# Kernel optimization log

Hardware: AMD Instinct MI355X
Metric: run time of the kernel (lower is better)

## Reference

```python
import jax, jax.numpy as jnp
import numpy as np

B, N, D, H, IN, HID = 16, 1024, 256, 8, 256, 1024
HD = IN // H  # head dim = 32
EPS = 1e-5


def layer_norm(x, g, b):
    mu = jnp.mean(x, axis=-1, keepdims=True)
    var = jnp.var(x, axis=-1, keepdims=True)
    return (x - mu) / jnp.sqrt(var + EPS) * g + b


def setup_inputs() -> dict:
    key = jax.random.key(0)
    ks = jax.random.split(key, 12)
    s = 0.02
    return {
        "x": jax.random.normal(ks[0], (B, N, D), jnp.float32),
        "coords": jax.random.normal(ks[1], (B, N, 2), jnp.float32),
        "g1": jnp.ones((D,), jnp.float32),
        "b1": jnp.zeros((D,), jnp.float32),
        "Wqkv": jax.random.normal(ks[2], (3 * IN, D), jnp.float32) * s,
        "Wproj": jax.random.normal(ks[3], (IN, IN), jnp.float32) * s,
        "bproj": jnp.zeros((IN,), jnp.float32),
        "g2": jnp.ones((D,), jnp.float32),
        "b2": jnp.zeros((D,), jnp.float32),
        "W1": jax.random.normal(ks[4], (HID, D), jnp.float32) * s,
        "bb1": jnp.zeros((HID,), jnp.float32),
        "W2": jax.random.normal(ks[5], (D, HID), jnp.float32) * s,
        "bb2": jnp.zeros((D,), jnp.float32),
    }


def reference(x, coords, g1, b1, Wqkv, Wproj, bproj, g2, b2, W1, bb1, W2, bb2):
    # ---- Attention branch (pre-norm) ----
    h = layer_norm(x, g1, b1)                       # [B,N,D]
    qkv = h @ Wqkv.T                                # [B,N,3*IN]
    qkv = qkv.reshape(B, N, 3, H, HD).transpose(2, 0, 3, 1, 4)  # [3,B,H,N,HD]
    q, k, v = qkv[0], qkv[1], qkv[2]
    scale = HD ** -0.5
    attn = jnp.einsum('bhid,bhjd->bhij', q * scale, k)  # [B,H,N,N]
    attn = jax.nn.softmax(attn, axis=-1)
    o = jnp.einsum('bhij,bhjd->bhid', attn, v)      # [B,H,N,HD]
    o = o.transpose(0, 2, 1, 3).reshape(B, N, IN)   # [B,N,IN]
    o = o @ Wproj.T + bproj
    o = o + h                                       # residual inside Attention (vs normed input)
    x = x + o                                       # Block residual (double residual, faithful)
    # ---- MLP branch ----
    h2 = layer_norm(x, g2, b2)
    m = jax.nn.gelu(h2 @ W1.T + bb1, approximate=False) @ W2.T + bb2
    return x + m
```

## Files before the change

kernel.cpp:

```cpp
#include <hip/hip_runtime.h>
#include <hip/hip_bf16.h>
#include <math.h>

#define Bdim 16
#define Ndim 1024
#define Ddim 256
#define Hdim 8
#define HDdim 32
#define INdim 256
#define HIDdim 1024
#define Tdim (Bdim * Ndim)

typedef __attribute__((ext_vector_type(8)))  short bf16x8;
typedef __attribute__((ext_vector_type(4)))  short bf16x4;
typedef __attribute__((ext_vector_type(16))) float f32x16;
typedef unsigned int u32;

__device__ inline short f2bf(float x) {
    union { __hip_bfloat16 b; short s; } u;
    u.b = __float2bfloat16(x);
    return u.s;
}

__device__ inline float bf2f(short s) {
    return __uint_as_float(((u32)(unsigned short)s) << 16);
}

__device__ inline float fexp2(float x) {
#if __has_builtin(__builtin_amdgcn_exp2f)
    return __builtin_amdgcn_exp2f(x);
#else
    return exp2f(x);
#endif
}

__device__ inline u32 pack2bf(float a, float b) {
#if __has_builtin(__builtin_amdgcn_cvt_pk_bf16_f32)
    typedef __attribute__((ext_vector_type(2))) __bf16 bf16x2_t;
    union { bf16x2_t v; u32 u; } c;
    c.v = __builtin_amdgcn_cvt_pk_bf16_f32(a, b);
    return c.u;
#else
    u32 ua = __float_as_uint(a), ub = __float_as_uint(b);
    return ((ua + 0x8000u) >> 16) | ((ub + 0x8000u) & 0xffff0000u);
#endif
}

__device__ inline void plswap(u32 &a, u32 &b) {
    asm volatile("v_permlane32_swap_b32 %0, %1" : "+v"(a), "+v"(b));
}

__device__ inline float gelu_exact(float v) {
    return 0.5f * v * (1.0f + erff(v * 0.70710678118654752f));
}

typedef __attribute__((address_space(1))) const u32 gas_t;
typedef __attribute__((address_space(3))) u32 las_t;
__device__ inline void gl16(const short* g, short* l) {
    __builtin_amdgcn_global_load_lds((gas_t*)g, (las_t*)l, 16, 0, 0);
}

#define N4_QKV  (3 * INdim * Ddim / 4)
#define N4_PROJ (INdim * INdim / 4)
#define N4_W1   (HIDdim * Ddim / 4)
#define N4_W2   (Ddim * HIDdim / 4)
#define NCVT_BLK ((N4_QKV + N4_PROJ + N4_W1 + N4_W2) / 256)

__global__ __launch_bounds__(256) void cvt_ln1_kernel(const float* __restrict__ s0,
                                                      const float* __restrict__ s1,
                                                      const float* __restrict__ s2,
                                                      const float* __restrict__ s3,
                                                      short* __restrict__ d0,
                                                      short* __restrict__ d1,
                                                      short* __restrict__ d2,
                                                      short* __restrict__ d3,
                                                      const float* __restrict__ x,
                                                      const float* __restrict__ g,
                                                      const float* __restrict__ b,
                                                      float* __restrict__ outf,
                                                      short* __restrict__ outb) {
    const int bid = blockIdx.x;
    if (bid < NCVT_BLK) {
        int i = bid * 256 + threadIdx.x;
        const float* src; short* dst; int j;
        if (i < N4_QKV)                          { src = s0; dst = d0; j = i; }
        else if (i < N4_QKV + N4_PROJ)           { src = s1; dst = d1; j = i - N4_QKV; }
        else if (i < N4_QKV + N4_PROJ + N4_W1)   { src = s2; dst = d2; j = i - N4_QKV - N4_PROJ; }
        else                                     { src = s3; dst = d3; j = i - N4_QKV - N4_PROJ - N4_W1; }
        float4 v = ((const float4*)src)[j];
        bf16x4 bb;
        bb[0] = f2bf(v.x); bb[1] = f2bf(v.y); bb[2] = f2bf(v.z); bb[3] = f2bf(v.w);
        ((bf16x4*)dst)[j] = bb;
    } else {
        int w = threadIdx.x >> 6, lane = threadIdx.x & 63;
        int row = (bid - NCVT_BLK) * 4 + w;
        float4 v = ((const float4*)x)[(size_t)row * 64 + lane];
        float s  = (v.x + v.y) + (v.z + v.w);
        float s2 = (v.x * v.x + v.y * v.y) + (v.z * v.z + v.w * v.w);
        #pragma unroll
        for (int off = 32; off; off >>= 1) {
            s  += __shfl_xor(s,  off, 64);
            s2 += __shfl_xor(s2, off, 64);
        }
        float mu   = s * (1.0f / Ddim);
        float var  = s2 * (1.0f / Ddim) - mu * mu;
        float rstd = rsqrtf(var + 1e-5f);
        float4 gg = ((const float4*)g)[lane];
        float4 bb = ((const float4*)b)[lane];
        float4 r;
        r.x = (v.x - mu) * rstd * gg.x + bb.x;
        r.y = (v.y - mu) * rstd * gg.y + bb.y;
        r.z = (v.z - mu) * rstd * gg.z + bb.z;
        r.w = (v.w - mu) * rstd * gg.w + bb.w;
        if (outf) ((float4*)outf)[(size_t)row * 64 + lane] = r;
        bf16x4 rb;
        rb[0] = f2bf(r.x); rb[1] = f2bf(r.y); rb[2] = f2bf(r.z); rb[3] = f2bf(r.w);
        ((bf16x4*)outb)[(size_t)row * 64 + lane] = rb;
    }
}

__global__ __launch_bounds__(256) void ln4_kernel(const float* __restrict__ x,
                                                  const float* __restrict__ g,
                                                  const float* __restrict__ b,
                                                  float* __restrict__ outf,
                                                  short* __restrict__ outb) {
    int w = threadIdx.x >> 6, lane = threadIdx.x & 63;
    int row = blockIdx.x * 4 + w;
    float4 v = ((const float4*)x)[(size_t)row * 64 + lane];
    float s  = (v.x + v.y) + (v.z + v.w);
    float s2 = (v.x * v.x + v.y * v.y) + (v.z * v.z + v.w * v.w);
    #pragma unroll
    for (int off = 32; off; off >>= 1) {
        s  += __shfl_xor(s,  off, 64);
        s2 += __shfl_xor(s2, off, 64);
    }
    float mu   = s * (1.0f / Ddim);
    float var  = s2 * (1.0f / Ddim) - mu * mu;
    float rstd = rsqrtf(var + 1e-5f);
    float4 gg = ((const float4*)g)[lane];
    float4 bb = ((const float4*)b)[lane];
    float4 r;
    r.x = (v.x - mu) * rstd * gg.x + bb.x;
    r.y = (v.y - mu) * rstd * gg.y + bb.y;
    r.z = (v.z - mu) * rstd * gg.z + bb.z;
    r.w = (v.w - mu) * rstd * gg.w + bb.w;
    if (outf) ((float4*)outf)[(size_t)row * 64 + lane] = r;
    bf16x4 rb;
    rb[0] = f2bf(r.x); rb[1] = f2bf(r.y); rb[2] = f2bf(r.z); rb[3] = f2bf(r.w);
    ((bf16x4*)outb)[(size_t)row * 64 + lane] = rb;
}

#define EPI_NONE 0
#define EPI_PROJ 1
#define EPI_GELU 2
#define EPI_RES  3
#define EPI_QKV  4

#define SCALE2Q 0.25505654249892417f

template <int EPI>
__global__ __launch_bounds__(256) void gemm128p(const short* __restrict__ A,
                                                const short* __restrict__ W,
                                                short* __restrict__ C,
                                                int N, int K,
                                                const float* __restrict__ bias) {
    __shared__ __attribute__((aligned(16))) short As[2][128 * 64];
    __shared__ __attribute__((aligned(16))) short Bs[2][128 * 64];
    const int tid = threadIdx.x, w = tid >> 6, lane = tid & 63;
    const int col = lane & 31;
    const int half_id = lane >> 5;

    const int nbx = gridDim.x;
    const int flat = blockIdx.y * nbx + blockIdx.x;
    const int cpx = (nbx * (int)gridDim.y) >> 3;
    const int swz = (flat & 7) * cpx + (flat >> 3);
    const int m0 = (swz / nbx) * 128, n0 = (swz % nbx) * 128;

    const int wm = (w & 1) * 64;
    const int wn = (w >> 1) * 64;

    f32x16 acc[2][2];
    #pragma unroll
    for (int i = 0; i < 2; ++i) { acc[i][0] = 0.0f; acc[i][1] = 0.0f; }

    const int lrow = lane >> 3;
    const int lchk = (lane & 7) ^ lrow;
    const short* gA = &A[(size_t)(m0 + w * 32 + lrow) * K + lchk * 8];
    const short* gB = &W[(size_t)(n0 + w * 32 + lrow) * K + lchk * 8];

    const int T = K >> 6;

    auto STAGE = [&](int buf, int kt) {
        short* lA = &As[buf][(w * 32) * 64];
        short* lB = &Bs[buf][(w * 32) * 64];
        #pragma unroll
        for (int i = 0; i < 4; ++i) {
            gl16(gA + (size_t)(i * 8) * K + kt * 64, lA + i * 512);
            gl16(gB + (size_t)(i * 8) * K + kt * 64, lB + i * 512);
        }
    };

    STAGE(0, 0);
    if (T > 1) {
        STAGE(1, 1);
        asm volatile("s_waitcnt vmcnt(8)" ::: "memory");
    } else {
        asm volatile("s_waitcnt vmcnt(0)" ::: "memory");
    }
    __builtin_amdgcn_s_barrier();

    for (int kt = 0; kt < T; ++kt) {
        const int buf = kt & 1;
        #pragma unroll
        for (int ks = 0; ks < 4; ++ks) {
            const int c = ks * 2 + half_id;
            bf16x8 af[2], bfv[2];
            #pragma unroll
            for (int t = 0; t < 2; ++t) {
                const int Ra = wm + t * 32 + col;
                af[t] = *(const bf16x8*)&As[buf][Ra * 64 + ((c ^ (Ra & 7)) * 8)];
                const int Rb = wn + t * 32 + col;
                bfv[t] = *(const bf16x8*)&Bs[buf][Rb * 64 + ((c ^ (Rb & 7)) * 8)];
            }
            #pragma unroll
            for (int tm = 0; tm < 2; ++tm)
                #pragma unroll
                for (int tn = 0; tn < 2; ++tn)
                    acc[tm][tn] = __builtin_amdgcn_mfma_f32_32x32x16_bf16(
                        af[tm], bfv[tn], acc[tm][tn], 0, 0, 0);
        }
        asm volatile("s_waitcnt lgkmcnt(0)" ::: "memory");
        __builtin_amdgcn_s_barrier();
        if (kt + 2 < T) {
            STAGE(buf, kt + 2);
            asm volatile("s_waitcnt vmcnt(8)" ::: "memory");
        } else {
            asm volatile("s_waitcnt vmcnt(0)" ::: "memory");
        }
        __builtin_amdgcn_s_barrier();
    }

    #pragma unroll
    for (int tm = 0; tm < 2; ++tm) {
        #pragma unroll
        for (int r = 0; r < 16; ++r) {
            int row = m0 + wm + tm * 32 + (r & 3) + 8 * (r >> 2) + 4 * half_id;
            #pragma unroll
            for (int tn = 0; tn < 2; ++tn) {
                int cn = n0 + wn + tn * 32 + col;
                float v = acc[tm][tn][r];
                if (EPI == EPI_QKV && cn < 256) v *= SCALE2Q;
                if (EPI == EPI_GELU) v = gelu_exact(v + bias[cn]);
                C[(size_t)row * N + cn] = f2bf(v);
            }
        }
    }
}

#define GPAD32 40

template <int EPI, int BN>
__global__ __launch_bounds__(256) void gemm_mfma(const short* __restrict__ A,
                                                 const short* __restrict__ W,
                                                 void* __restrict__ Cv,
                                                 int M, int N, int K,
                                                 const float* __restrict__ bias,
                                                 const float* __restrict__ add1,
                                                 const float* __restrict__ add2) {
    __shared__ short As[64 * GPAD32];
    __shared__ short Bs[BN * GPAD32];
    const int tid = threadIdx.x, w = tid >> 6, lane = tid & 63;
    const int col = lane & 31;
    const int half_id = lane >> 5;

    const int nbx = gridDim.x;
    const int flat = blockIdx.y * nbx + blockIdx.x;
    const int cpx = (nbx * (int)gridDim.y) >> 3;
    const int swz = (flat & 7) * cpx + (flat >> 3);
    const int m0 = (swz / nbx) * 64, n0 = (swz % nbx) * BN;

    const int wm = (w & 1) * 32;
    const int wn = (BN == 128) ? (w >> 1) * 64 : (w >> 1) * 32;
    constexpr int TN = (BN == 128) ? 2 : 1;

    f32x16 acc[TN];
    #pragma unroll
    for (int t = 0; t < TN; ++t) acc[t] = 0.0f;

    const int sra = tid >> 2, ssa = (tid & 3) * 8;
    const int srb = (BN == 128) ? (tid >> 1) : (tid >> 2);
    const int ssb = (BN == 128) ? (tid & 1) * 16 : (tid & 3) * 8;
    constexpr int NB = (BN == 128) ? 2 : 1;

    const short* pAsrc = &A[(size_t)(m0 + sra) * K + ssa];
    const short* pBsrc = &W[(size_t)(n0 + srb) * K + ssb];

    bf16x8 pa, pb[NB];
    pa = *(const bf16x8*)&pAsrc[0];
    #pragma unroll
    for (int j = 0; j < NB; ++j) pb[j] = *(const bf16x8*)&pBsrc[j * 8];

    const int T = K >> 5;
    for (int kt = 0; kt < T; ++kt) {
        __syncthreads();
        *(bf16x8*)&As[sra * GPAD32 + ssa] = pa;
        #pragma unroll
        for (int j = 0; j < NB; ++j) *(bf16x8*)&Bs[srb * GPAD32 + ssb + j * 8] = pb[j];
        __syncthreads();

        if (kt + 1 < T) {
            const short* a = pAsrc + (kt + 1) * 32;
            const short* b = pBsrc + (kt + 1) * 32;
            pa = *(const bf16x8*)&a[0];
            #pragma unroll
            for (int j = 0; j < NB; ++j) pb[j] = *(const bf16x8*)&b[j * 8];
        }

        #pragma unroll
        for (int ks = 0; ks < 2; ++ks) {
            bf16x8 af = *(const bf16x8*)&As[(wm + col) * GPAD32 + ks * 16 + half_id * 8];
            bf16x8 bfv[TN];
            #pragma unroll
            for (int t = 0; t < TN; ++t)
                bfv[t] = *(const bf16x8*)&Bs[(wn + t * 32 + col) * GPAD32 + ks * 16 + half_id * 8];
            #pragma unroll
            for (int t = 0; t < TN; ++t)
                acc[t] = __builtin_amdgcn_mfma_f32_32x32x16_bf16(af, bfv[t], acc[t], 0, 0, 0);
        }
    }

    float* Cf = (float*)Cv;
    short* Cb = (short*)Cv;
    #pragma unroll
    for (int r = 0; r < 16; ++r) {
        int row = m0 + wm + (r & 3) + 8 * (r >> 2) + 4 * half_id;
        #pragma unroll
        for (int t = 0; t < TN; ++t) {
            int cn = n0 + wn + t * 32 + col;
            size_t off = (size_t)row * N + cn;
            float v = acc[t][r];
            if (EPI != EPI_NONE && EPI != EPI_QKV) v += bias[cn];
            if (EPI == EPI_GELU) v = gelu_exact(v);
            if (EPI == EPI_PROJ) v += add1[off] + add2[off];
            if (EPI == EPI_RES)  v += add1[off];
            if (EPI == EPI_PROJ || EPI == EPI_RES) Cf[off] = v;
            else                                   Cb[off] = f2bf(v);
        }
    }
}

#define VTPAD 136

__global__ __launch_bounds__(256) void vtrans_kernel(const short* __restrict__ qkv,
                                                     short* __restrict__ vT) {
    __shared__ short Tl[32 * VTPAD];
    const int tid = threadIdx.x;
    const int bh = blockIdx.x, c = blockIdx.y;
    const int b = bh >> 3, head = bh & 7;
    {
        int r = tid >> 1, hv = tid & 1;
        const short* src = qkv + (size_t)b * Ndim * 768 + (size_t)(c * 128 + r) * 768
                           + 512 + head * 32 + hv * 16;
        bf16x8 v0 = *(const bf16x8*)&src[0];
        bf16x8 v1 = *(const bf16x8*)&src[8];
        #pragma unroll
        for (int i = 0; i < 8; ++i) {
            Tl[(hv * 16 + i) * VTPAD + r]     = v0[i];
            Tl[(hv * 16 + 8 + i) * VTPAD + r] = v1[i];
        }
    }
    __syncthreads();
    {
        int d = tid >> 3, j16 = (tid & 7) * 16;
        short* dst = vT + (size_t)(bh * 32 + d) * Ndim + c * 128 + j16;
        *(bf16x8*)&dst[0] = *(const bf16x8*)&Tl[d * VTPAD + j16];
        *(bf16x8*)&dst[8] = *(const bf16x8*)&Tl[d * VTPAD + j16 + 8];
    }
}

#define KVPAD 40
#define CHUNK 128

__global__ __launch_bounds__(256) void attn_mfma_kernel(const short* __restrict__ qkv,
                                                        const short* __restrict__ vT,
                                                        short* __restrict__ oat) {
    __shared__ short Ks[CHUNK * KVPAD];
    __shared__ short Vt[32 * VTPAD];

    const int tid = threadIdx.x;
    const int w = tid >> 6;
    const int lane = tid & 63;
    const int col = lane & 31;
    const int half_id = lane >> 5;

    const int id = blockIdx.x;
    const int xcd = id & 7;
    const int s_ = id >> 3;
    const int bh = ((s_ >> 3) << 3) | xcd;
    const int qblk = s_ & 7;

    const int b = bh >> 3, head = bh & 7;
    const int q0w = qblk * 128 + w * 32;

    const size_t qkvb = (size_t)b * Ndim * 768;

    const int sr = tid >> 1, shv = tid & 1;
    const short* ksrc = qkv + qkvb + (size_t)sr * 768 + 256 + head * 32 + shv * 16;
    const int sd = tid >> 3, sj16 = (tid & 7) * 16;
    const short* vsrc = vT + (size_t)(bh * 32 + sd) * Ndim + sj16;

    bf16x8 qf[2];
    {
        const short* qrow = qkv + qkvb + (size_t)(q0w + col) * 768 + head * 32;
        #pragma unroll
        for (int kh = 0; kh < 2; ++kh)
            qf[kh] = *(const bf16x8*)&qrow[kh * 16 + half_id * 8];
    }

    bf16x8 vone;
    #pragma unroll
    for (int i = 0; i < 8; ++i) vone[i] = (short)0x3F80;

    f32x16 o_acc = 0.0f, l_acc = 0.0f;

    bf16x8 rk0, rk1, rv0, rv1;
    {
        rk0 = *(const bf16x8*)&ksrc[0];
        rk1 = *(const bf16x8*)&ksrc[8];
        rv0 = *(const bf16x8*)&vsrc[0];
        rv1 = *(const bf16x8*)&vsrc[8];
    }

    for (int ci = 0; ci < 8; ++ci) {
        if (ci != 0) __syncthreads();
        *(bf16x8*)&Ks[sr * KVPAD + shv * 16]     = rk0;
        *(bf16x8*)&Ks[sr * KVPAD + shv * 16 + 8] = rk1;
        *(bf16x8*)&Vt[sd * VTPAD + sj16]     = rv0;
        *(bf16x8*)&Vt[sd * VTPAD + sj16 + 8] = rv1;
        __syncthreads();

        if (ci < 7) {
            const short* kp = ksrc + (size_t)((ci + 1) * CHUNK) * 768;
            rk0 = *(const bf16x8*)&kp[0];
            rk1 = *(const bf16x8*)&kp[8];
            const short* vp = vsrc + (ci + 1) * CHUNK;
            rv0 = *(const bf16x8*)&vp[0];
            rv1 = *(const bf16x8*)&vp[8];
        }

        f32x16 s_cur;
        {
            bf16x8 kf0 = *(bf16x8*)&Ks[col * KVPAD + half_id * 8];
            bf16x8 kf1 = *(bf16x8*)&Ks[col * KVPAD + 16 + half_id * 8];
            f32x16 z = 0.0f;
            z = __builtin_amdgcn_mfma_f32_32x32x16_bf16(kf0, qf[0], z, 0, 0, 0);
            z = __builtin_amdgcn_mfma_f32_32x32x16_bf16(kf1, qf[1], z, 0, 0, 0);
            s_cur = z;
        }
        #pragma unroll
        for (int jt = 0; jt < 4; ++jt) {
            f32x16 s_next;
            if (jt < 3) {
                bf16x8 kf0 = *(bf16x8*)&Ks[((jt + 1) * 32 + col) * KVPAD + half_id * 8];
                bf16x8 kf1 = *(bf16x8*)&Ks[((jt + 1) * 32 + col) * KVPAD + 16 + half_id * 8];
                f32x16 z = 0.0f;
                z = __builtin_amdgcn_mfma_f32_32x32x16_bf16(kf0, qf[0], z, 0, 0, 0);
                z = __builtin_amdgcn_mfma_f32_32x32x16_bf16(kf1, qf[1], z, 0, 0, 0);
                s_next = z;
            }

            bf16x8 vf0 = *(bf16x8*)&Vt[col * VTPAD + jt * 32 + half_id * 8];
            bf16x8 vf1 = *(bf16x8*)&Vt[col * VTPAD + jt * 32 + 16 + half_id * 8];

            u32 wd[8];
            #pragma unroll
            for (int g = 0; g < 8; ++g) {
                float e0 = fexp2(s_cur[2 * g + 0]);
                float e1 = fexp2(s_cur[2 * g + 1]);
                wd[g] = pack2bf(e0, e1);
            }
            plswap(wd[0], wd[2]); plswap(wd[1], wd[3]);
            plswap(wd[4], wd[6]); plswap(wd[5], wd[7]);

            union { u32 u[4]; bf16x8 v; } p0, p1;
            p0.u[0] = wd[0]; p0.u[1] = wd[1]; p0.u[2] = wd[2]; p0.u[3] = wd[3];
            p1.u[0] = wd[4]; p1.u[1] = wd[5]; p1.u[2] = wd[6]; p1.u[3] = wd[7];

            __builtin_amdgcn_s_setprio(1);
            o_acc = __builtin_amdgcn_mfma_f32_32x32x16_bf16(p0.v, vf0, o_acc, 0, 0, 0);
            o_acc = __builtin_amdgcn_mfma_f32_32x32x16_bf16(p1.v, vf1, o_acc, 0, 0, 0);
            l_acc = __builtin_amdgcn_mfma_f32_32x32x16_bf16(p0.v, vone, l_acc, 0, 0, 0);
            l_acc = __builtin_amdgcn_mfma_f32_32x32x16_bf16(p1.v, vone, l_acc, 0, 0, 0);
            __builtin_amdgcn_s_setprio(0);

            if (jt < 3) s_cur = s_next;
        }
    }

    #pragma unroll
    for (int r = 0; r < 16; ++r) {
        int q_r = (r & 3) + 8 * (r >> 2) + 4 * half_id;
        size_t gq = (size_t)(b * Ndim + q0w + q_r);
        oat[gq * INdim + head * 32 + col] = f2bf(o_acc[r] / l_acc[r]);
    }
}

extern "C" void kernel_launch(void* const* d_in, const int* in_sizes, int n_in,
                              void* d_out, int out_size, void* d_ws, size_t ws_size,
                              hipStream_t stream) {
    const float* x     = (const float*)d_in[0];
    const float* g1    = (const float*)d_in[2];
    const float* b1    = (const float*)d_in[3];
    const float* Wqkv  = (const float*)d_in[4];
    const float* Wproj = (const float*)d_in[5];
    const float* bproj = (const float*)d_in[6];
    const float* g2    = (const float*)d_in[7];
    const float* b2    = (const float*)d_in[8];
    const float* W1    = (const float*)d_in[9];
    const float* bb1   = (const float*)d_in[10];
    const float* W2    = (const float*)d_in[11];
    const float* bb2   = (const float*)d_in[12];
    float* out = (float*)d_out;

    char* ws = (char*)d_ws;
    float* h      = (float*)(ws);
    short* h_bf   = (short*)(ws + (size_t)(16u << 20));
    short* qkv_bf = (short*)(ws + (size_t)(24u << 20));
    float* xnew   = (float*)(ws + (size_t)(24u << 20));
    short* oat_bf = (short*)(ws + (size_t)(48u << 20));
    short* mid_bf = (short*)(ws + (size_t)(56u << 20));
    short* vT     = (short*)(ws + (size_t)(81u << 20));
    short* wqkv_b = (short*)(ws + (size_t)(89u << 20));
    short* wproj_b= (short*)(ws + (size_t)(89u << 20) + 768 * 1024);
    short* w1_b   = (short*)(ws + (size_t)(90u << 20));
    short* w2_b   = (short*)(ws + (size_t)(90u << 20) + 512 * 1024);

    cvt_ln1_kernel<<<NCVT_BLK + Tdim / 4, 256, 0, stream>>>(
        Wqkv, Wproj, W1, W2, wqkv_b, wproj_b, w1_b, w2_b,
        x, g1, b1, h, h_bf);
    gemm128p<EPI_QKV><<<dim3(768 / 128, Tdim / 128), 256, 0, stream>>>(
        h_bf, wqkv_b, qkv_bf, 768, 256, nullptr);
    vtrans_kernel<<<dim3(Bdim * Hdim, Ndim / 128), 256, 0, stream>>>(qkv_bf, vT);
    attn_mfma_kernel<<<1024, 256, 0, stream>>>(qkv_bf, vT, oat_bf);
    gemm_mfma<EPI_PROJ, 64><<<dim3(256 / 64, Tdim / 64), 256, 0, stream>>>(
        oat_bf, wproj_b, xnew, Tdim, 256, 256, bproj, h, x);
    ln4_kernel<<<Tdim / 4, 256, 0, stream>>>(xnew, g2, b2, nullptr, h_bf);
    gemm128p<EPI_GELU><<<dim3(1024 / 128, Tdim / 128), 256, 0, stream>>>(
        h_bf, w1_b, mid_bf, 1024, 256, bb1);
    gemm_mfma<EPI_RES, 64><<<dim3(256 / 64, Tdim / 64), 256, 0, stream>>>(
        mid_bf, w2_b, out, Tdim, 256, 1024, bb2, xnew, nullptr);
}
```

Measured before the change: 208.0 us.

## Compute V transposed directly via swapped-operand GEMM; use 128-tile GEMM for MLP down-proj

Removes the separate V transpose kernel by computing V^T per batch as a GEMM of the V weight rows against the normalized activations, writing the [head*dim, N] layout that attention consumes. The QKV GEMM now produces only Q and K with a 512-wide row stride, and attention indexing is updated to match. It also moves the final MLP down-projection (K=1024) from the 64-tile GEMM to the double-buffered 128-tile GEMM, with a fused bias-plus-residual fp32 epilogue. This saves a kernel launch and a round trip of V through memory, but the down-projection now runs on only 256 blocks, which may leave the GPU's compute units underused.

```diff
diff --git a/kernel.cpp b/kernel.cpp
--- a/kernel.cpp
+++ b/kernel.cpp
@@ -155,20 +155,30 @@
 #define EPI_GELU 2
 #define EPI_RES  3
 #define EPI_QKV  4
+#define EPI_VT   5
 
 #define SCALE2Q 0.25505654249892417f
 
 template <int EPI>
 __global__ __launch_bounds__(256) void gemm128p(const short* __restrict__ A,
-                                                const short* __restrict__ W,
-                                                short* __restrict__ C,
+                                                const short* __restrict__ Wp,
+                                                void* __restrict__ Cv,
                                                 int N, int K,
-                                                const float* __restrict__ bias) {
+                                                const float* __restrict__ bias,
+                                                const float* __restrict__ add1) {
     __shared__ __attribute__((aligned(16))) short As[2][128 * 64];
     __shared__ __attribute__((aligned(16))) short Bs[2][128 * 64];
     const int tid = threadIdx.x, w = tid >> 6, lane = tid & 63;
     const int col = lane & 31;
     const int half_id = lane >> 5;
+
+    const short* W = Wp;
+    short* Cb = (short*)Cv;
+    float* Cf = (float*)Cv;
+    if constexpr (EPI == EPI_VT) {
+        W  += (size_t)blockIdx.z * Ndim * Ddim;
+        Cb += (size_t)blockIdx.z * 256 * Ndim;
+    }
 
     const int nbx = gridDim.x;
     const int flat = blockIdx.y * nbx + blockIdx.x;
@@ -248,10 +258,12 @@
             #pragma unroll
             for (int tn = 0; tn < 2; ++tn) {
                 int cn = n0 + wn + tn * 32 + col;
+                size_t off = (size_t)row * N + cn;
                 float v = acc[tm][tn][r];
                 if (EPI == EPI_QKV && cn < 256) v *= SCALE2Q;
                 if (EPI == EPI_GELU) v = gelu_exact(v + bias[cn]);
-                C[(size_t)row * N + cn] = f2bf(v);
+                if (EPI == EPI_RES)  Cf[off] = v + bias[cn] + add1[off];
+                else                 Cb[off] = f2bf(v);
             }
         }
     }
@@ -349,39 +361,11 @@
     }
 }
 
-#define VTPAD 136
-
-__global__ __launch_bounds__(256) void vtrans_kernel(const short* __restrict__ qkv,
-                                                     short* __restrict__ vT) {
-    __shared__ short Tl[32 * VTPAD];
-    const int tid = threadIdx.x;
-    const int bh = blockIdx.x, c = blockIdx.y;
-    const int b = bh >> 3, head = bh & 7;
-    {
-        int r = tid >> 1, hv = tid & 1;
-        const short* src = qkv + (size_t)b * Ndim * 768 + (size_t)(c * 128 + r) * 768
-                           + 512 + head * 32 + hv * 16;
-        bf16x8 v0 = *(const bf16x8*)&src[0];
-        bf16x8 v1 = *(const bf16x8*)&src[8];
-        #pragma unroll
-        for (int i = 0; i < 8; ++i) {
-            Tl[(hv * 16 + i) * VTPAD + r]     = v0[i];
-            Tl[(hv * 16 + 8 + i) * VTPAD + r] = v1[i];
-        }
-    }
-    __syncthreads();
-    {
-        int d = tid >> 3, j16 = (tid & 7) * 16;
-        short* dst = vT + (size_t)(bh * 32 + d) * Ndim + c * 128 + j16;
-        *(bf16x8*)&dst[0] = *(const bf16x8*)&Tl[d * VTPAD + j16];
-        *(bf16x8*)&dst[8] = *(const bf16x8*)&Tl[d * VTPAD + j16 + 8];
-    }
-}
-
 #define KVPAD 40
 #define CHUNK 128
-
-__global__ __launch_bounds__(256) void attn_mfma_kernel(const short* __restrict__ qkv,
+#define VTPAD 136
+
+__global__ __launch_bounds__(256) void attn_mfma_kernel(const short* __restrict__ qk,
                                                         const short* __restrict__ vT,
                                                         short* __restrict__ oat) {
     __shared__ short Ks[CHUNK * KVPAD];
@@ -402,16 +386,16 @@
     const int b = bh >> 3, head = bh & 7;
     const int q0w = qblk * 128 + w * 32;
 
-    const size_t qkvb = (size_t)b * Ndim * 768;
+    const size_t qkb = (size_t)b * Ndim * 512;
 
     const int sr = tid >> 1, shv = tid & 1;
-    const short* ksrc = qkv + qkvb + (size_t)sr * 768 + 256 + head * 32 + shv * 16;
+    const short* ksrc = qk + qkb + (size_t)sr * 512 + 256 + head * 32 + shv * 16;
     const int sd = tid >> 3, sj16 = (tid & 7) * 16;
     const short* vsrc = vT + (size_t)(bh * 32 + sd) * Ndim + sj16;
 
     bf16x8 qf[2];
     {
-        const short* qrow = qkv + qkvb + (size_t)(q0w + col) * 768 + head * 32;
+        const short* qrow = qk + qkb + (size_t)(q0w + col) * 512 + head * 32;
         #pragma unroll
         for (int kh = 0; kh < 2; ++kh)
             qf[kh] = *(const bf16x8*)&qrow[kh * 16 + half_id * 8];
@@ -440,7 +424,7 @@
         __syncthreads();
 
         if (ci < 7) {
-            const short* kp = ksrc + (size_t)((ci + 1) * CHUNK) * 768;
+            const short* kp = ksrc + (size_t)((ci + 1) * CHUNK) * 512;
             rk0 = *(const bf16x8*)&kp[0];
             rk1 = *(const bf16x8*)&kp[8];
             const short* vp = vsrc + (ci + 1) * CHUNK;
@@ -525,7 +509,7 @@
     char* ws = (char*)d_ws;
     float* h      = (float*)(ws);
     short* h_bf   = (short*)(ws + (size_t)(16u << 20));
-    short* qkv_bf = (short*)(ws + (size_t)(24u << 20));
+    short* qk_bf  = (short*)(ws + (size_t)(24u << 20));
     float* xnew   = (float*)(ws + (size_t)(24u << 20));
     short* oat_bf = (short*)(ws + (size_t)(48u << 20));
     short* mid_bf = (short*)(ws + (size_t)(56u << 20));
@@ -534,19 +518,21 @@
     short* wproj_b= (short*)(ws + (size_t)(89u << 20) + 768 * 1024);
     short* w1_b   = (short*)(ws + (size_t)(90u << 20));
     short* w2_b   = (short*)(ws + (size_t)(90u << 20) + 512 * 1024);
+    short* wv_b   = wqkv_b + 512 * 256;
 
     cvt_ln1_kernel<<<NCVT_BLK + Tdim / 4, 256, 0, stream>>>(
         Wqkv, Wproj, W1, W2, wqkv_b, wproj_b, w1_b, w2_b,
         x, g1, b1, h, h_bf);
-    gemm128p<EPI_QKV><<<dim3(768 / 128, Tdim / 128), 256, 0, stream>>>(
-        h_bf, wqkv_b, qkv_bf, 768, 256, nullptr);
-    vtrans_kernel<<<dim3(Bdim * Hdim, Ndim / 128), 256, 0, stream>>>(qkv_bf, vT);
-    attn_mfma_kernel<<<1024, 256, 0, stream>>>(qkv_bf, vT, oat_bf);
+    gemm128p<EPI_QKV><<<dim3(512 / 128, Tdim / 128), 256, 0, stream>>>(
+        h_bf, wqkv_b, qk_bf, 512, 256, nullptr, nullptr);
+    gemm128p<EPI_VT><<<dim3(Ndim / 128, 256 / 128, Bdim), 256, 0, stream>>>(
+        wv_b, h_bf, vT, Ndim, 256, nullptr, nullptr);
+    attn_mfma_kernel<<<1024, 256, 0, stream>>>(qk_bf, vT, oat_bf);
     gemm_mfma<EPI_PROJ, 64><<<dim3(256 / 64, Tdim / 64), 256, 0, stream>>>(
         oat_bf, wproj_b, xnew, Tdim, 256, 256, bproj, h, x);
     ln4_kernel<<<Tdim / 4, 256, 0, stream>>>(xnew, g2, b2, nullptr, h_bf);
     gemm128p<EPI_GELU><<<dim3(1024 / 128, Tdim / 128), 256, 0, stream>>>(
-        h_bf, w1_b, mid_bf, 1024, 256, bb1);
-    gemm_mfma<EPI_RES, 64><<<dim3(256 / 64, Tdim / 64), 256, 0, stream>>>(
-        mid_bf, w2_b, out, Tdim, 256, 1024, bb2, xnew, nullptr);
-}
+        h_bf, w1_b, mid_bf, 1024, 256, bb1, nullptr);
+    gemm128p<EPI_RES><<<dim3(256 / 128, Tdim / 128), 256, 0, stream>>>(
+        mid_bf, w2_b, out, 256, 1024, bb2, xnew);
+}
```

Measured after the change: 205.6 us (median of 2 runs). Within noise of the previous version (-1.1%).
